# Kernel optimization log

Measured on AMD Instinct MI355X. Metric: run time of the kernel, lower is better.

The kernel has to match this reference:

```python
import jax, jax.numpy as jnp
import numpy as np

MINI_BLOCK = 4

def setup_inputs() -> dict:
    key = jax.random.key(0)
    k1, k2 = jax.random.split(key)
    B, IN, OUT = 4096, 4096, 4096
    gy, gx = OUT // MINI_BLOCK, IN // MINI_BLOCK
    x = jax.random.normal(k1, (B, IN), dtype=jnp.float32)
    eigens = jax.random.normal(k2, (gy, gx, MINI_BLOCK), dtype=jnp.float32)
    return {"x": x, "eigens": eigens}

def reference(x, eigens):
    # Block-circulant linear: out[b, y, :] = sum_x circconv(eigens[y, x], x_blk[b, x])
    # computed in the frequency domain. Original code used two-sided rfft +
    # complex_mult + irfft per (b, y, x) block and summed over x; since the FFT
    # and complex product are linear, we contract over x in frequency space
    # with an einsum instead of materializing the (B, gy, gx, block) tensor.
    gy, gx, blk = eigens.shape
    xb = x.reshape(-1, gx, blk)                      # (B, gx, blk)
    f_eig = jnp.fft.rfft(eigens, axis=-1)            # (gy, gx, blk//2+1) complex
    f_x = jnp.fft.rfft(xb, axis=-1)                  # (B, gx, blk//2+1)
    f_out = jnp.einsum('yxk,bxk->byk', f_eig, f_x)   # contract over gx
    out = jnp.fft.irfft(f_out, n=blk, axis=-1)       # (B, gy, blk)
    return out.reshape(-1, gy * blk)
```

## Files before the change

kernel.cpp:

```cpp
#include <hip/hip_runtime.h>


typedef __attribute__((ext_vector_type(8))) short bf16x8_t;
typedef __attribute__((ext_vector_type(4))) float f32x4_t;

#define NDIM 4096
#define TILE 128
#define BK 32

__device__ __forceinline__ unsigned short f2bf(float f) {
    unsigned int u = __builtin_bit_cast(unsigned int, f);
    u += 0x7fffu + ((u >> 16) & 1u);
    return (unsigned short)(u >> 16);
}

__device__ __forceinline__ void async_copy16(const void* g, void* l) {
    __builtin_amdgcn_global_load_lds(
        (const __attribute__((address_space(1))) void*)g,
        (__attribute__((address_space(3))) void*)l,
        16, 0, 0);
}


__global__ __launch_bounds__(256) void pre_k(const float* __restrict__ x,
                                             const float* __restrict__ eig,
                                             unsigned short* __restrict__ xp,
                                             unsigned short* __restrict__ B) {
    const int t = threadIdx.x;
    if (blockIdx.x < 4096) {
        int gid = blockIdx.x * 256 + t;
        int b = gid >> 8, j0 = (gid & 255) << 2;
        const float4* src = (const float4*)x + ((size_t)b << 10) + j0;
        unsigned short S[4], R[4], Mi[4], Z[4], T[4];
#pragma unroll
        for (int q = 0; q < 4; ++q) {
            float4 v = src[q];
            float r = v.x - v.z, m = v.w - v.y;
            S[q]  = f2bf(r + m);
            R[q]  = f2bf(r);
            Mi[q] = f2bf(m);
            Z[q]  = f2bf(v.x + v.y + v.z + v.w);
            T[q]  = f2bf(v.x - v.y + v.z - v.w);
        }
        unsigned short* dst = xp + (size_t)b * 5120 + j0;
        *(ushort4*)(dst)        = *(const ushort4*)S;
        *(ushort4*)(dst + 1024) = *(const ushort4*)R;
        *(ushort4*)(dst + 2048) = *(const ushort4*)Mi;
        *(ushort4*)(dst + 3072) = *(const ushort4*)Z;
        *(ushort4*)(dst + 4096) = *(const ushort4*)T;
    } else {
        int gid = (blockIdx.x - 4096) * 256 + t;
        int y = gid >> 8, c0 = (gid & 255) << 2;
        const float4* src = (const float4*)eig + ((size_t)y << 10) + c0;
        unsigned short P0[4], P1[4], P2[4], P3[4], P4[4];
#pragma unroll
        for (int q = 0; q < 4; ++q) {
            float4 v = src[q];
            float r = v.x - v.z, m = v.w - v.y;
            P0[q] = f2bf(r);
            P1[q] = f2bf(m - r);
            P2[q] = f2bf(-(m + r));
            P3[q] = f2bf(v.x + v.y + v.z + v.w);
            P4[q] = f2bf(v.x - v.y + v.z - v.w);
        }
        unsigned short* dst = B + (size_t)y * 5120 + c0;
        *(ushort4*)(dst)        = *(const ushort4*)P0;
        *(ushort4*)(dst + 1024) = *(const ushort4*)P1;
        *(ushort4*)(dst + 2048) = *(const ushort4*)P2;
        *(ushort4*)(dst + 3072) = *(const ushort4*)P3;
        *(ushort4*)(dst + 4096) = *(const ushort4*)P4;
    }
}

__global__ __launch_bounds__(256, 1) void gemm_f(
        const unsigned short* __restrict__ A,
        const unsigned short* __restrict__ B,
        float* __restrict__ C) {
    __shared__ unsigned short sm[3][16384];

    const int raw    = blockIdx.x;
    const int xcd    = raw & 7;
    const int idx    = raw >> 3;
    const int rowBlk = xcd * 4 + (idx >> 3);
    const int colBlk = idx & 7;

    const int t    = threadIdx.x;
    const int lane = t & 63;
    const int w    = t >> 6;
    const int wm   = (w >> 1) * 64;
    const int wn   = (w & 1) * 64;
    const int lr   = lane & 15;
    const int quad = lane >> 4;
    const int xr   = lr & 7;

    const int srow = t >> 3;
    const int scol = ((t & 7) ^ (srow & 7)) << 3;
    const unsigned short* paw = A + (size_t)(rowBlk * 128 + srow) * 5120 + scol;
    const unsigned short* pbw = B + (size_t)(colBlk * 128 + srow) * 5120 + scol;
    const unsigned short* pa0 = paw;
    const unsigned short* pa1 = paw + (size_t)32 * 5120;
    const unsigned short* pa2 = paw + (size_t)64 * 5120;
    const unsigned short* pa3 = paw + (size_t)96 * 5120;
    const unsigned short* pb0 = pbw;
    const unsigned short* pb1 = pbw + (size_t)32 * 5120;
    const unsigned short* pb2 = pbw + (size_t)64 * 5120;
    const unsigned short* pb3 = pbw + (size_t)96 * 5120;

    char* smb  = (char*)&sm[0][0];
    char* dstT = smb + srow * 128 + (t & 7) * 16;

    int koff = 0;

    f32x4_t accA[4][4] = {};
    f32x4_t accB[4][4] = {};

#define STAGE4(BOFF)                                           \
    {                                                          \
        char* d = dstT + (BOFF);                               \
        async_copy16(pa0 + koff, d);                           \
        async_copy16(pa1 + koff, d + 4096);                    \
        async_copy16(pa2 + koff, d + 8192);                    \
        async_copy16(pa3 + koff, d + 12288);                   \
        async_copy16(pb0 + koff, d + 16384);                   \
        async_copy16(pb1 + koff, d + 20480);                   \
        async_copy16(pb2 + koff, d + 24576);                   \
        async_copy16(pb3 + koff, d + 28672);                   \
        koff += 64;                                            \
    }

#define COMPUTE4(BOFF, ACC)                                                   \
    {                                                                         \
        const char* ab = smb + (BOFF) + (wm + lr) * 128;                      \
        const char* bb = smb + (BOFF) + 16384 + (wn + lr) * 128;              \
        _Pragma("unroll")                                                     \
        for (int kk = 0; kk < 2; ++kk) {                                      \
            const int sw = ((((kk << 2) | quad)) ^ xr) << 4;                  \
            bf16x8_t af[4], bfv[4];                                           \
            _Pragma("unroll")                                                 \
            for (int i = 0; i < 4; ++i)                                       \
                af[i] = *(const bf16x8_t*)(ab + i * 2048 + sw);               \
            _Pragma("unroll")                                                 \
            for (int j = 0; j < 4; ++j)                                       \
                bfv[j] = *(const bf16x8_t*)(bb + j * 2048 + sw);              \
            __builtin_amdgcn_s_setprio(1);                                    \
            _Pragma("unroll")                                                 \
            for (int mt = 0; mt < 4; ++mt)                                    \
                _Pragma("unroll")                                             \
                for (int nt = 0; nt < 4; ++nt)                                \
                    ACC[mt][nt] = __builtin_amdgcn_mfma_f32_16x16x32_bf16(    \
                        af[mt], bfv[nt], ACC[mt][nt], 0, 0, 0);               \
            __builtin_amdgcn_s_setprio(0);                                    \
        }                                                                     \
    }

#define STEP4(ACC)                                             \
    {                                                          \
        asm volatile("s_waitcnt vmcnt(8)" ::: "memory");       \
        __builtin_amdgcn_s_barrier();                          \
        __builtin_amdgcn_sched_barrier(0);                     \
        int sb_ = cb + 65536;                                  \
        if (sb_ >= 98304) sb_ -= 98304;                        \
        if (koff < 5120) STAGE4(sb_);                          \
        COMPUTE4(cb, ACC);                                     \
        cb += 32768;                                           \
        if (cb >= 98304) cb = 0;                               \
    }

#define PHASE4(ACC, NSTEP)                                     \
    _Pragma("unroll 1")                                        \
    for (int s2 = 0; s2 < (NSTEP); ++s2) STEP4(ACC)

    STAGE4(0);
    STAGE4(32768);
    int cb = 0;

    PHASE4(accA, 16)
#pragma unroll
    for (int mt = 0; mt < 4; ++mt)
#pragma unroll
        for (int nt = 0; nt < 4; ++nt) accB[mt][nt] = accA[mt][nt];
    PHASE4(accB, 16)
    PHASE4(accA, 16)

    const int prow0   = rowBlk * 128 + wm + quad * 4;
    const int colBase = colBlk * 512;
    const int lc      = wn + lr;
#pragma unroll
    for (int mt = 0; mt < 4; ++mt) {
#pragma unroll
        for (int r = 0; r < 4; ++r) {
            float* pr = C + (size_t)(prow0 + mt * 16 + r) * NDIM + colBase;
#pragma unroll
            for (int nt = 0; nt < 4; ++nt) {
                pr[lc + nt * 16]       = accA[mt][nt][r];
                pr[128 + lc + nt * 16] = accB[mt][nt][r];
            }
        }
    }
    {
        f32x4_t z = {0.f, 0.f, 0.f, 0.f};
#pragma unroll
        for (int mt = 0; mt < 4; ++mt)
#pragma unroll
            for (int nt = 0; nt < 4; ++nt) { accA[mt][nt] = z; accB[mt][nt] = z; }
    }

    PHASE4(accA, 16)
    PHASE4(accB, 15)

    asm volatile("s_waitcnt vmcnt(0)" ::: "memory");
    __builtin_amdgcn_s_barrier();
    __builtin_amdgcn_sched_barrier(0);
    COMPUTE4(cb, accB);

#undef PHASE4
#undef STEP4
#undef COMPUTE4
#undef STAGE4

    float por[4][4][4], poi[4][4][4];
#pragma unroll
    for (int mt = 0; mt < 4; ++mt) {
#pragma unroll
        for (int r = 0; r < 4; ++r) {
            const float* pr = C + (size_t)(prow0 + mt * 16 + r) * NDIM + colBase;
#pragma unroll
            for (int nt = 0; nt < 4; ++nt) {
                por[mt][nt][r] = pr[lc + nt * 16];
                poi[mt][nt][r] = pr[128 + lc + nt * 16];
            }
        }
    }
    asm volatile("s_waitcnt vmcnt(0)" ::: "memory");
    __builtin_amdgcn_s_barrier();

#pragma unroll
    for (int mt = 0; mt < 4; ++mt) {
#pragma unroll
        for (int r = 0; r < 4; ++r) {
            float* dst = C + (size_t)(prow0 + mt * 16 + r) * NDIM;
#pragma unroll
            for (int nt = 0; nt < 4; ++nt) {
                int yc = colBlk * 128 + wn + nt * 16 + lr;
                float O0 = accA[mt][nt][r], O2 = accB[mt][nt][r];
                float Or = por[mt][nt][r], Oi = poi[mt][nt][r];
                float4 o;
                o.x = 0.25f * (O0 + 2.0f * Or + O2);
                o.y = 0.25f * (O0 - 2.0f * Oi - O2);
                o.z = 0.25f * (O0 - 2.0f * Or + O2);
                o.w = 0.25f * (O0 + 2.0f * Oi - O2);
                *(float4*)(dst + 4 * yc) = o;
            }
        }
    }
}


__global__ __launch_bounds__(256) void fwd_x_fb(const float* __restrict__ x,
                                                unsigned short* __restrict__ xp) {
    int gid = blockIdx.x * 256 + threadIdx.x;
    int b = gid >> 10, j = gid & 1023;
    float4 v = ((const float4*)x)[(size_t)b * 1024 + j];
    unsigned short* dst = xp + (size_t)b * NDIM + j;
    dst[0]    = f2bf(v.x + v.y + v.z + v.w);
    dst[1024] = f2bf(v.x - v.z);
    dst[2048] = f2bf(v.w - v.y);
    dst[3072] = f2bf(v.x - v.y + v.z - v.w);
}

__global__ __launch_bounds__(256) void build_b_fb(const float* __restrict__ eig,
                                                  unsigned short* __restrict__ B) {
    int gid = blockIdx.x * 256 + threadIdx.x;
    int y = gid >> 10, c = gid & 1023;
    float4 v = ((const float4*)eig)[(size_t)y * 1024 + c];
    float r = v.x - v.z, s = v.w - v.y;
    B[(size_t)y * 1024 + c] = f2bf(v.x + v.y + v.z + v.w);
    unsigned short* b1r = B + 1048576 + (size_t)y * 2048;
    b1r[c]        = f2bf(r);
    b1r[1024 + c] = f2bf(-s);
    unsigned short* b1i = B + 3145728 + (size_t)y * 2048;
    b1i[c]        = f2bf(s);
    b1i[1024 + c] = f2bf(r);
    B[5242880 + (size_t)y * 1024 + c] = f2bf(v.x - v.y + v.z - v.w);
}

__global__ __launch_bounds__(256, 2) void gemm_fb(
        const unsigned short* __restrict__ A,
        const unsigned short* __restrict__ B,
        float* __restrict__ C) {
    __shared__ unsigned short lA[TILE * BK];
    __shared__ unsigned short lB[TILE * BK];

    const int Ks[4]   = {1024, 2048, 2048, 1024};
    const int Aoff[4] = {0, 1024, 1024, 3072};
    const size_t Boff[4] = {0u, 1048576u, 3145728u, 5242880u};

    int lin = blockIdx.x;
    int seg, nseg, blkM;
    if (lin < 512) { seg = 1 + ((lin >> 3) & 1); nseg = lin & 7; blkM = lin >> 4; }
    else { int i = lin - 512; seg = ((i >> 3) & 1) * 3; nseg = i & 7; blkM = i >> 4; }

    const int K    = Ks[seg];
    const int aoff = Aoff[seg];
    const unsigned short* Bs = B + Boff[seg];

    const int t    = threadIdx.x;
    const int lane = t & 63;
    const int w    = t >> 6;
    const int wm   = (w >> 1) * 64;
    const int wn   = (w & 1) * 64;
    const int lr   = lane & 15;
    const int quad = lane >> 4;

    const int e0 = t * 8;
    const int r0 = e0 >> 5;
    const int c0 = e0 & 31;

    const unsigned short* pa0 = A + (size_t)(blkM * TILE + r0) * NDIM + aoff + c0;
    const unsigned short* pa1 = pa0 + (size_t)64 * NDIM;
    const unsigned short* pb0 = Bs + (size_t)(nseg * TILE + r0) * K + c0;
    const unsigned short* pb1 = pb0 + (size_t)64 * K;

    unsigned short* dA0 = &lA[e0];
    unsigned short* dA1 = &lA[2048 + e0];
    unsigned short* dB0 = &lB[e0];
    unsigned short* dB1 = &lB[2048 + e0];

    const unsigned short* la0 = &lA[(wm + lr) * BK + quad * 8];
    const unsigned short* lb0 = &lB[(wn + lr) * BK + quad * 8];

    f32x4_t acc[4][4] = {};

    for (int k0 = 0; k0 < K; k0 += BK) {
        async_copy16(pa0 + k0, dA0);
        async_copy16(pa1 + k0, dA1);
        async_copy16(pb0 + k0, dB0);
        async_copy16(pb1 + k0, dB1);
        asm volatile("s_waitcnt vmcnt(0)" ::: "memory");
        __syncthreads();

        bf16x8_t af[4], bfr[4];
#pragma unroll
        for (int i = 0; i < 4; ++i)
            af[i] = *(const bf16x8_t*)(la0 + i * 16 * BK);
#pragma unroll
        for (int i = 0; i < 4; ++i)
            bfr[i] = *(const bf16x8_t*)(lb0 + i * 16 * BK);

#pragma unroll
        for (int mt = 0; mt < 4; ++mt)
#pragma unroll
            for (int nt = 0; nt < 4; ++nt)
                acc[mt][nt] = __builtin_amdgcn_mfma_f32_16x16x32_bf16(
                    af[mt], bfr[nt], acc[mt][nt], 0, 0, 0);

        __syncthreads();
    }

    const int orow0 = blkM * TILE + wm + quad * 4;
    const int ocol0 = seg * 1024 + nseg * TILE + wn + lr;
#pragma unroll
    for (int mt = 0; mt < 4; ++mt) {
#pragma unroll
        for (int r = 0; r < 4; ++r) {
            float* dst = C + (size_t)(orow0 + mt * 16 + r) * NDIM + ocol0;
#pragma unroll
            for (int nt = 0; nt < 4; ++nt)
                dst[nt * 16] = acc[mt][nt][r];
        }
    }
}

__global__ __launch_bounds__(256) void post_fb(float* __restrict__ O) {
    float* row = O + (size_t)blockIdx.x * NDIM;
    const int t = threadIdx.x;
    float4 v0 = *(const float4*)(row + 4 * t);
    float4 vr = *(const float4*)(row + 1024 + 4 * t);
    float4 vi = *(const float4*)(row + 2048 + 4 * t);
    float4 v2 = *(const float4*)(row + 3072 + 4 * t);
    __syncthreads();
    const float* a0 = (const float*)&v0;
    const float* ar = (const float*)&vr;
    const float* ai = (const float*)&vi;
    const float* a2 = (const float*)&v2;
#pragma unroll
    for (int i = 0; i < 4; ++i) {
        float4 o;
        o.x = 0.25f * (a0[i] + 2.0f * ar[i] + a2[i]);
        o.y = 0.25f * (a0[i] - 2.0f * ai[i] - a2[i]);
        o.z = 0.25f * (a0[i] - 2.0f * ar[i] + a2[i]);
        o.w = 0.25f * (a0[i] + 2.0f * ai[i] - a2[i]);
        *(float4*)(row + 16 * t + 4 * i) = o;
    }
}


extern "C" void kernel_launch(void* const* d_in, const int* in_sizes, int n_in,
                              void* d_out, int out_size, void* d_ws, size_t ws_size,
                              hipStream_t stream) {
    const float* x   = (const float*)d_in[0];
    const float* eig = (const float*)d_in[1];
    float* out = (float*)d_out;

    const size_t NEED = (size_t)50 * 1024 * 1024;

    if (ws_size >= NEED) {
        unsigned short* Xp = (unsigned short*)d_ws;
        unsigned short* Bp = (unsigned short*)((char*)d_ws + 41943040u);

        pre_k<<<5120, 256, 0, stream>>>(x, eig, Xp, Bp);
        gemm_f<<<256, 256, 0, stream>>>(Xp, Bp, out);
    } else {
        unsigned short* Xp = (unsigned short*)d_ws;
        unsigned short* Bp = Xp + (size_t)NDIM * NDIM;

        fwd_x_fb<<<(NDIM * 1024) / 256, 256, 0, stream>>>(x, Xp);
        build_b_fb<<<(1024 * 1024) / 256, 256, 0, stream>>>(eig, Bp);
        gemm_fb<<<dim3(1024, 1), 256, 0, stream>>>(Xp, Bp, out);
        post_fb<<<NDIM, 256, 0, stream>>>(out);
    }
}
```

Baseline: 190.6 us.

## Give each wave private LDS double buffers and drop block barriers in GEMM

The block-shared triple-buffered LDS staging, where each wave cooperatively loads the whole 128x64 A/B tile, is replaced with per-wave private double buffers. Each wave now async-loads only its own 64-row A and B slices. Because no wave reads another wave's data, all s_barrier calls are removed and synchronisation relies only on vmcnt waits. The cost is that A and B rows are loaded twice, since two waves share each, doubling global/L2 traffic into LDS and raising LDS usage to 128KB.

Measured after the change: 194.9 us. +2.3%, slower.

```diff
diff --git a/kernel.cpp b/kernel.cpp
--- a/kernel.cpp
+++ b/kernel.cpp
@@ -76,7 +76,7 @@
         const unsigned short* __restrict__ A,
         const unsigned short* __restrict__ B,
         float* __restrict__ C) {
-    __shared__ unsigned short sm[3][16384];
+    __shared__ char smem[4][32768];
 
     const int raw    = blockIdx.x;
     const int xcd    = raw & 7;
@@ -87,51 +87,46 @@
     const int t    = threadIdx.x;
     const int lane = t & 63;
     const int w    = t >> 6;
-    const int wm   = (w >> 1) * 64;
-    const int wn   = (w & 1) * 64;
     const int lr   = lane & 15;
     const int quad = lane >> 4;
     const int xr   = lr & 7;
 
-    const int srow = t >> 3;
-    const int scol = ((t & 7) ^ (srow & 7)) << 3;
-    const unsigned short* paw = A + (size_t)(rowBlk * 128 + srow) * 5120 + scol;
-    const unsigned short* pbw = B + (size_t)(colBlk * 128 + srow) * 5120 + scol;
-    const unsigned short* pa0 = paw;
-    const unsigned short* pa1 = paw + (size_t)32 * 5120;
-    const unsigned short* pa2 = paw + (size_t)64 * 5120;
-    const unsigned short* pa3 = paw + (size_t)96 * 5120;
-    const unsigned short* pb0 = pbw;
-    const unsigned short* pb1 = pbw + (size_t)32 * 5120;
-    const unsigned short* pb2 = pbw + (size_t)64 * 5120;
-    const unsigned short* pb3 = pbw + (size_t)96 * 5120;
-
-    char* smb  = (char*)&sm[0][0];
-    char* dstT = smb + srow * 128 + (t & 7) * 16;
+    const int wrow  = rowBlk * 128 + (w >> 1) * 64;
+    const int wcolY = colBlk * 128 + (w & 1) * 64;
+
+    const int sj = lane >> 3;
+    const int sc = (lane & 7) ^ sj;
+    const unsigned short* pa = A + (size_t)(wrow + sj) * 5120 + sc * 8;
+    const unsigned short* pb = B + (size_t)(wcolY + sj) * 5120 + sc * 8;
+
+    char* smw = &smem[w][0];
+    char* dA  = smw + lane * 16;
+    char* dB  = smw + 8192 + lane * 16;
 
     int koff = 0;
+    int cb   = 0;
 
     f32x4_t accA[4][4] = {};
     f32x4_t accB[4][4] = {};
 
-#define STAGE4(BOFF)                                           \
-    {                                                          \
-        char* d = dstT + (BOFF);                               \
-        async_copy16(pa0 + koff, d);                           \
-        async_copy16(pa1 + koff, d + 4096);                    \
-        async_copy16(pa2 + koff, d + 8192);                    \
-        async_copy16(pa3 + koff, d + 12288);                   \
-        async_copy16(pb0 + koff, d + 16384);                   \
-        async_copy16(pb1 + koff, d + 20480);                   \
-        async_copy16(pb2 + koff, d + 24576);                   \
-        async_copy16(pb3 + koff, d + 28672);                   \
-        koff += 64;                                            \
-    }
-
-#define COMPUTE4(BOFF, ACC)                                                   \
+#define STAGE_P(BUF)                                                     \
+    {                                                                    \
+        const unsigned short* pak = pa + koff;                           \
+        const unsigned short* pbk = pb + koff;                           \
+        char* da = dA + (BUF) * 16384;                                   \
+        char* db = dB + (BUF) * 16384;                                   \
+        _Pragma("unroll")                                                \
+        for (int j = 0; j < 8; ++j) {                                    \
+            async_copy16(pak + (size_t)j * 40960, da + j * 1024);        \
+            async_copy16(pbk + (size_t)j * 40960, db + j * 1024);        \
+        }                                                                \
+        koff += 64;                                                      \
+    }
+
+#define COMPUTE_P(BUF, ACC)                                                   \
     {                                                                         \
-        const char* ab = smb + (BOFF) + (wm + lr) * 128;                      \
-        const char* bb = smb + (BOFF) + 16384 + (wn + lr) * 128;              \
+        const char* ab = smw + (BUF) * 16384 + lr * 128;                      \
+        const char* bb = smw + (BUF) * 16384 + 8192 + lr * 128;               \
         _Pragma("unroll")                                                     \
         for (int kk = 0; kk < 2; ++kk) {                                      \
             const int sw = ((((kk << 2) | quad)) ^ xr) << 4;                  \
@@ -153,50 +148,45 @@
         }                                                                     \
     }
 
-#define STEP4(ACC)                                             \
+#define STEP_P(ACC)                                            \
     {                                                          \
-        asm volatile("s_waitcnt vmcnt(8)" ::: "memory");       \
-        __builtin_amdgcn_s_barrier();                          \
+        asm volatile("s_waitcnt vmcnt(16)" ::: "memory");      \
         __builtin_amdgcn_sched_barrier(0);                     \
-        int sb_ = cb + 65536;                                  \
-        if (sb_ >= 98304) sb_ -= 98304;                        \
-        if (koff < 5120) STAGE4(sb_);                          \
-        COMPUTE4(cb, ACC);                                     \
-        cb += 32768;                                           \
-        if (cb >= 98304) cb = 0;                               \
-    }
-
-#define PHASE4(ACC, NSTEP)                                     \
+        COMPUTE_P(cb, ACC);                                    \
+        __builtin_amdgcn_sched_barrier(0);                     \
+        if (koff < 5120) STAGE_P(cb);                          \
+        cb ^= 1;                                               \
+    }
+
+#define PHASE_P(ACC, NSTEP)                                    \
     _Pragma("unroll 1")                                        \
-    for (int s2 = 0; s2 < (NSTEP); ++s2) STEP4(ACC)
-
-    STAGE4(0);
-    STAGE4(32768);
-    int cb = 0;
-
-    PHASE4(accA, 16)
+    for (int s2 = 0; s2 < (NSTEP); ++s2) STEP_P(ACC)
+
+    STAGE_P(0);
+    STAGE_P(1);
+
+    PHASE_P(accA, 16)
 #pragma unroll
     for (int mt = 0; mt < 4; ++mt)
 #pragma unroll
         for (int nt = 0; nt < 4; ++nt) accB[mt][nt] = accA[mt][nt];
-    PHASE4(accB, 16)
-    PHASE4(accA, 16)
-
-    const int prow0   = rowBlk * 128 + wm + quad * 4;
-    const int colBase = colBlk * 512;
-    const int lc      = wn + lr;
+    PHASE_P(accB, 16)
+    PHASE_P(accA, 16)
+
 #pragma unroll
     for (int mt = 0; mt < 4; ++mt) {
 #pragma unroll
         for (int r = 0; r < 4; ++r) {
-            float* pr = C + (size_t)(prow0 + mt * 16 + r) * NDIM + colBase;
+            float* pr = C + (size_t)(wrow + mt * 16 + quad * 4 + r) * NDIM +
+                        wcolY * 4;
 #pragma unroll
             for (int nt = 0; nt < 4; ++nt) {
-                pr[lc + nt * 16]       = accA[mt][nt][r];
-                pr[128 + lc + nt * 16] = accB[mt][nt][r];
+                pr[nt * 16 + lr]      = accA[mt][nt][r];
+                pr[64 + nt * 16 + lr] = accB[mt][nt][r];
             }
         }
     }
+    asm volatile("s_waitcnt vmcnt(0)" ::: "memory");
     {
         f32x4_t z = {0.f, 0.f, 0.f, 0.f};
 #pragma unroll
@@ -205,43 +195,42 @@
             for (int nt = 0; nt < 4; ++nt) { accA[mt][nt] = z; accB[mt][nt] = z; }
     }
 
-    PHASE4(accA, 16)
-    PHASE4(accB, 15)
+    PHASE_P(accA, 16)
+    PHASE_P(accB, 15)
 
     asm volatile("s_waitcnt vmcnt(0)" ::: "memory");
-    __builtin_amdgcn_s_barrier();
     __builtin_amdgcn_sched_barrier(0);
-    COMPUTE4(cb, accB);
-
-#undef PHASE4
-#undef STEP4
-#undef COMPUTE4
-#undef STAGE4
+    COMPUTE_P(cb, accB);
+
+#undef PHASE_P
+#undef STEP_P
+#undef COMPUTE_P
+#undef STAGE_P
 
     float por[4][4][4], poi[4][4][4];
 #pragma unroll
     for (int mt = 0; mt < 4; ++mt) {
 #pragma unroll
         for (int r = 0; r < 4; ++r) {
-            const float* pr = C + (size_t)(prow0 + mt * 16 + r) * NDIM + colBase;
+            const float* pr = C + (size_t)(wrow + mt * 16 + quad * 4 + r) * NDIM +
+                              wcolY * 4;
 #pragma unroll
             for (int nt = 0; nt < 4; ++nt) {
-                por[mt][nt][r] = pr[lc + nt * 16];
-                poi[mt][nt][r] = pr[128 + lc + nt * 16];
+                por[mt][nt][r] = pr[nt * 16 + lr];
+                poi[mt][nt][r] = pr[64 + nt * 16 + lr];
             }
         }
     }
     asm volatile("s_waitcnt vmcnt(0)" ::: "memory");
-    __builtin_amdgcn_s_barrier();
 
 #pragma unroll
     for (int mt = 0; mt < 4; ++mt) {
 #pragma unroll
         for (int r = 0; r < 4; ++r) {
-            float* dst = C + (size_t)(prow0 + mt * 16 + r) * NDIM;
+            float* dst = C + (size_t)(wrow + mt * 16 + quad * 4 + r) * NDIM;
 #pragma unroll
             for (int nt = 0; nt < 4; ++nt) {
-                int yc = colBlk * 128 + wn + nt * 16 + lr;
+                int yc = wcolY + nt * 16 + lr;
                 float O0 = accA[mt][nt][r], O2 = accB[mt][nt][r];
                 float Or = por[mt][nt][r], Oi = poi[mt][nt][r];
                 float4 o;
```
